# Performance work log

Measured on AMD Instinct MI355X. Metric: run time of the kernel, lower is better.

Reference implementation:

```python
import jax, jax.numpy as jnp
import numpy as np


def _pairwise_sqdist(x, y):
    # x: [B, N, 3], y: [B, M, 3] -> squared L2 distances [B, N, M]
    x2 = jnp.sum(x * x, axis=-1)  # [B, N]
    y2 = jnp.sum(y * y, axis=-1)  # [B, M]
    xy = jnp.einsum('bnd,bmd->bnm', x, y)  # [B, N, M]
    d2 = x2[:, :, None] + y2[:, None, :] - 2.0 * xy
    return jnp.maximum(d2, 0.0)


def setup_inputs() -> dict:
    key = jax.random.key(0)
    kx, ky = jax.random.split(key)
    B, N, M, D = 4, 4096, 4096, 3
    x = jax.random.normal(kx, (B, N, D), dtype=jnp.float32)
    y = jax.random.normal(ky, (B, M, D), dtype=jnp.float32)
    return {"x": x, "y": y}


def reference(x, y):
    # Single-directional chamfer, pytorch3d defaults:
    # squared-L2 NN dist, mean over points, mean over batch -> scalar.
    d2 = _pairwise_sqdist(x, y)  # [B, N, M]
    # x -> y: for each x point, min over y points
    x_to_y = jnp.mean(jnp.min(d2, axis=2))
    # y -> x: for each y point, min over x points (reuse same matrix)
    y_to_x = jnp.mean(jnp.min(d2, axis=1))
    return jnp.maximum(x_to_y, y_to_x)
```

## Files before the change

### kernel.cpp

```cpp
#include <hip/hip_runtime.h>

#define B_      4
#define N_      4096
#define BN_     (B_ * N_)
#define TPB     256
#define SCAN_SL 256
#define OWN_SL  512
#define ONE_BF  0x3F80u


typedef __attribute__((ext_vector_type(8)))  short bf16x8;
typedef __attribute__((ext_vector_type(16))) float f32x16;

__device__ __forceinline__ unsigned bf16_rne(float f) {
    unsigned u = __float_as_uint(f);
    u += 0x7FFFu + ((u >> 16) & 1u);
    return u >> 16;
}

__global__ __launch_bounds__(TPB) void chamfer_kernel(
    const float* __restrict__ x, const float* __restrict__ y,
    int* __restrict__ mins)
{
    __shared__ __align__(16) unsigned sA[SCAN_SL * 8];
    __shared__ __align__(16) unsigned sB[OWN_SL * 8];

    const int tid = threadIdx.x;
    const int z   = blockIdx.z;
    const int b   = z & (B_ - 1);
    const int dir = z >> 2;
    const float* ownp = dir ? y : x;
    const float* scnp = dir ? x : y;
    int* omin = mins + dir * BN_ + b * N_;

    const int scan_base = blockIdx.x * SCAN_SL;
    const int own_base  = blockIdx.y * OWN_SL;

    {
        const float* s = scnp + ((size_t)b * N_ + scan_base + tid) * 3;
        const float s0 = s[0], s1 = s[1], s2 = s[2];
        const float ss = 0.5f * (s0 * s0 + s1 * s1 + s2 * s2);
        unsigned h0 = bf16_rne(s0), h1 = bf16_rne(s1), h2 = bf16_rne(s2);
        unsigned l0 = bf16_rne(s0 - __uint_as_float(h0 << 16));
        unsigned l1 = bf16_rne(s1 - __uint_as_float(h1 << 16));
        unsigned l2 = bf16_rne(s2 - __uint_as_float(h2 << 16));
        unsigned sh = bf16_rne(ss);
        unsigned sl = bf16_rne(ss - __uint_as_float(sh << 16));
        h0 ^= 0x8000u; h1 ^= 0x8000u; h2 ^= 0x8000u;
        l0 ^= 0x8000u; l1 ^= 0x8000u; l2 ^= 0x8000u;
        unsigned* a = &sA[tid * 8];
        const unsigned w0 = h0 | (h1 << 16);
        const unsigned w1 = h2 | (l0 << 16);
        const unsigned w2 = l1 | (l2 << 16);
        a[0] = w0; a[1] = w1; a[2] = w2;
        a[3] = w0; a[4] = w1; a[5] = w2;
        a[6] = sh | (sl << 16);
        a[7] = ONE_BF | (ONE_BF << 16);
    }
    #pragma unroll
    for (int r = 0; r < 2; ++r) {
        const int o = tid + r * TPB;
        const float* q = ownp + ((size_t)b * N_ + own_base + o) * 3;
        const float q0 = q[0], q1 = q[1], q2 = q[2];
        const float qq = 0.5f * (q0 * q0 + q1 * q1 + q2 * q2);
        const unsigned h0 = bf16_rne(q0), h1 = bf16_rne(q1), h2 = bf16_rne(q2);
        const unsigned l0 = bf16_rne(q0 - __uint_as_float(h0 << 16));
        const unsigned l1 = bf16_rne(q1 - __uint_as_float(h1 << 16));
        const unsigned l2 = bf16_rne(q2 - __uint_as_float(h2 << 16));
        const unsigned qh = bf16_rne(qq);
        const unsigned ql = bf16_rne(qq - __uint_as_float(qh << 16));
        unsigned* p = &sB[o * 8];
        p[0] = h0 | (h1 << 16);
        p[1] = h2 | (h0 << 16);
        p[2] = h1 | (h2 << 16);
        p[3] = l0 | (l1 << 16);
        p[4] = l2 | (l0 << 16);
        p[5] = l1 | (l2 << 16);
        p[6] = ONE_BF | (ONE_BF << 16);
        p[7] = qh | (ql << 16);
    }
    __syncthreads();

    const int w  = tid >> 6;
    const int ln = tid & 31;
    const int lq = (tid >> 5) & 1;

    bf16x8 bfr[4];
    #pragma unroll
    for (int t = 0; t < 4; ++t)
        bfr[t] = *(const bf16x8*)&sB[((w * 4 + t) * 32 + ln) * 8 + lq * 4];

    float c[4] = {3.4e38f, 3.4e38f, 3.4e38f, 3.4e38f};

    const f32x16 fzero = {};

    #pragma unroll 2
    for (int st = 0; st < SCAN_SL / 32; ++st) {
        const bf16x8 af = *(const bf16x8*)&sA[(st * 32 + ln) * 8 + lq * 4];
        #pragma unroll
        for (int t = 0; t < 4; ++t) {
            const f32x16 acc =
                __builtin_amdgcn_mfma_f32_32x32x16_bf16(af, bfr[t], fzero,
                                                        0, 0, 0);
            const float u0 = fminf(fminf(acc[0],  acc[1]),  acc[2]);
            const float u1 = fminf(fminf(acc[3],  acc[4]),  acc[5]);
            const float u2 = fminf(fminf(acc[6],  acc[7]),  acc[8]);
            const float u3 = fminf(fminf(acc[9],  acc[10]), acc[11]);
            const float u4 = fminf(fminf(acc[12], acc[13]), acc[14]);
            const float v0 = fminf(fminf(u0, u1), acc[15]);
            const float v1 = fminf(fminf(u2, u3), u4);
            c[t] = fminf(c[t], fminf(v0, v1));
        }
    }

    #pragma unroll
    for (int t = 0; t < 4; ++t) {
        const float d2 = fmaxf(c[t] * 2.0f, 0.0f);
        atomicMax(&omin[own_base + (w * 4 + t) * 32 + ln],
                  -__float_as_int(d2));
    }
}

__global__ __launch_bounds__(1024) void finalize_kernel(
    const int* __restrict__ mins, float* __restrict__ out)
{
    const int tid = threadIdx.x;
    const int4* m4 = (const int4*)mins;
    float s0 = 0.0f, s1 = 0.0f;
    #pragma unroll
    for (int i = 0; i < BN_ / 4; i += 1024) {
        const int4 a = m4[i + tid];
        s0 += __int_as_float(-a.x) + __int_as_float(-a.y)
            + __int_as_float(-a.z) + __int_as_float(-a.w);
        const int4 c = m4[BN_ / 4 + i + tid];
        s1 += __int_as_float(-c.x) + __int_as_float(-c.y)
            + __int_as_float(-c.z) + __int_as_float(-c.w);
    }
    #pragma unroll
    for (int o = 32; o > 0; o >>= 1) {
        s0 += __shfl_down(s0, o);
        s1 += __shfl_down(s1, o);
    }
    __shared__ float w0[16], w1[16];
    const int w = tid >> 6;
    if ((tid & 63) == 0) { w0[w] = s0; w1[w] = s1; }
    __syncthreads();
    if (tid == 0) {
        float t0 = 0.0f, t1 = 0.0f;
        #pragma unroll
        for (int i = 0; i < 16; ++i) { t0 += w0[i]; t1 += w1[i]; }
        const float inv = 1.0f / (float)BN_;
        out[0] = fmaxf(t0 * inv, t1 * inv);
    }
}

extern "C" void kernel_launch(void* const* d_in, const int* in_sizes, int n_in,
                              void* d_out, int out_size, void* d_ws, size_t ws_size,
                              hipStream_t stream)
{
    const float* x = (const float*)d_in[0];
    const float* y = (const float*)d_in[1];
    float* out = (float*)d_out;

    int* mins = (int*)d_ws;

    dim3 grid(N_ / SCAN_SL, N_ / OWN_SL, 2 * B_);
    chamfer_kernel<<<grid, TPB, 0, stream>>>(x, y, mins);

    finalize_kernel<<<1, 1024, 0, stream>>>(mins, out);
}
```

Baseline: 66.91 us.

## Replace atomic min reduction with per-slice partial minima and multi-block finalize

Each chamfer block now folds its two half-waves with a cross-lane shuffle and writes plain stores into its own partial-minimum slice, instead of issuing atomicMax on a shared minimum array. The finalize step becomes eight blocks, one per direction and batch, that take the min across the 16 slices and sum. A small third kernel combines these eight sums. This drops atomic contention and any need to pre-initialize the minimum buffer, at the cost of roughly 2 MB of extra workspace traffic and one more kernel launch.

```diff
diff --git a/kernel.cpp b/kernel.cpp
--- a/kernel.cpp
+++ b/kernel.cpp
@@ -6,6 +6,7 @@
 #define TPB     256
 #define SCAN_SL 256
 #define OWN_SL  512
+#define NSLICE  (N_ / SCAN_SL)
 #define ONE_BF  0x3F80u
 
 
@@ -20,7 +21,7 @@
 
 __global__ __launch_bounds__(TPB) void chamfer_kernel(
     const float* __restrict__ x, const float* __restrict__ y,
-    int* __restrict__ mins)
+    float* __restrict__ pmin)
 {
     __shared__ __align__(16) unsigned sA[SCAN_SL * 8];
     __shared__ __align__(16) unsigned sB[OWN_SL * 8];
@@ -31,7 +32,6 @@
     const int dir = z >> 2;
     const float* ownp = dir ? y : x;
     const float* scnp = dir ? x : y;
-    int* omin = mins + dir * BN_ + b * N_;
 
     const int scan_base = blockIdx.x * SCAN_SL;
     const int own_base  = blockIdx.y * OWN_SL;
@@ -113,44 +113,58 @@
         }
     }
 
+    float m32[4];
     #pragma unroll
-    for (int t = 0; t < 4; ++t) {
-        const float d2 = fmaxf(c[t] * 2.0f, 0.0f);
-        atomicMax(&omin[own_base + (w * 4 + t) * 32 + ln],
-                  -__float_as_int(d2));
+    for (int t = 0; t < 4; ++t)
+        m32[t] = fminf(c[t], __shfl_xor(c[t], 32));
+
+    float* pslice = pmin +
+        ((((size_t)dir * B_ + b) * NSLICE + blockIdx.x) * N_) + own_base;
+    if (!(tid & 32)) {
+        #pragma unroll
+        for (int t = 0; t < 4; ++t)
+            pslice[(w * 4 + t) * 32 + ln] = m32[t] * 2.0f;
     }
 }
 
 __global__ __launch_bounds__(1024) void finalize_kernel(
-    const int* __restrict__ mins, float* __restrict__ out)
+    const float* __restrict__ pmin, float* __restrict__ bsums)
 {
+    const int blk = blockIdx.x;
+    const float* base = pmin + (size_t)blk * NSLICE * N_;
     const int tid = threadIdx.x;
-    const int4* m4 = (const int4*)mins;
-    float s0 = 0.0f, s1 = 0.0f;
+
+    float s = 0.0f;
     #pragma unroll
-    for (int i = 0; i < BN_ / 4; i += 1024) {
-        const int4 a = m4[i + tid];
-        s0 += __int_as_float(-a.x) + __int_as_float(-a.y)
-            + __int_as_float(-a.z) + __int_as_float(-a.w);
-        const int4 c = m4[BN_ / 4 + i + tid];
-        s1 += __int_as_float(-c.x) + __int_as_float(-c.y)
-            + __int_as_float(-c.z) + __int_as_float(-c.w);
+    for (int k = 0; k < N_ / 1024; ++k) {
+        const int n = k * 1024 + tid;
+        float m = base[n];
+        #pragma unroll
+        for (int sl = 1; sl < NSLICE; ++sl)
+            m = fminf(m, base[sl * N_ + n]);
+        s += fmaxf(m, 0.0f);
     }
     #pragma unroll
-    for (int o = 32; o > 0; o >>= 1) {
-        s0 += __shfl_down(s0, o);
-        s1 += __shfl_down(s1, o);
-    }
-    __shared__ float w0[16], w1[16];
-    const int w = tid >> 6;
-    if ((tid & 63) == 0) { w0[w] = s0; w1[w] = s1; }
+    for (int o = 32; o > 0; o >>= 1)
+        s += __shfl_down(s, o);
+    __shared__ float ws[16];
+    if ((tid & 63) == 0) ws[tid >> 6] = s;
     __syncthreads();
     if (tid == 0) {
-        float t0 = 0.0f, t1 = 0.0f;
+        float t0 = 0.0f;
         #pragma unroll
-        for (int i = 0; i < 16; ++i) { t0 += w0[i]; t1 += w1[i]; }
-        const float inv = 1.0f / (float)BN_;
-        out[0] = fmaxf(t0 * inv, t1 * inv);
+        for (int i = 0; i < 16; ++i) t0 += ws[i];
+        bsums[blk] = t0;
+    }
+}
+
+__global__ __launch_bounds__(64) void combine_kernel(
+    const float* __restrict__ bsums, float* __restrict__ out)
+{
+    if (threadIdx.x == 0) {
+        const float s0 = bsums[0] + bsums[1] + bsums[2] + bsums[3];
+        const float s1 = bsums[4] + bsums[5] + bsums[6] + bsums[7];
+        out[0] = fmaxf(s0, s1) * (1.0f / (float)BN_);
     }
 }
 
@@ -162,10 +176,12 @@
     const float* y = (const float*)d_in[1];
     float* out = (float*)d_out;
 
-    int* mins = (int*)d_ws;
+    float* pmin  = (float*)d_ws;
+    float* bsums = pmin + (size_t)2 * B_ * NSLICE * N_;
 
-    dim3 grid(N_ / SCAN_SL, N_ / OWN_SL, 2 * B_);
-    chamfer_kernel<<<grid, TPB, 0, stream>>>(x, y, mins);
+    dim3 grid(NSLICE, N_ / OWN_SL, 2 * B_);
+    chamfer_kernel<<<grid, TPB, 0, stream>>>(x, y, pmin);
 
-    finalize_kernel<<<1, 1024, 0, stream>>>(mins, out);
+    finalize_kernel<<<2 * B_, 1024, 0, stream>>>(pmin, bsums);
+    combine_kernel<<<1, 64, 0, stream>>>(bsums, out);
 }
```

Result: slower. 68.95 us (+3.1%).
